# Kernel optimization log

Hardware: AMD Instinct MI355X
Metric: run time of the kernel (lower is better)

## Reference

```python
import jax, jax.numpy as jnp
import numpy as np

NUM_CLASSES = 100000
NUM_SAMPLED = 5000  # num_classes * cr, cr = 0.05
BATCH = 4096
DIM = 1024


def _log_expected_count(idx, num_sampled, num_classes):
    # TF LogUniformCandidateSampler: P(c) = log((c+2)/(c+1)) / log(num_classes+1)
    c = idx.astype(jnp.float32)
    p = jnp.log((c + 2.0) / (c + 1.0)) / jnp.log(float(num_classes) + 1.0)
    # expected count for unique sampling of num_sampled candidates
    return jnp.log(-jnp.expm1(num_sampled * jnp.log1p(-p)))


def setup_inputs() -> dict:
    key = jax.random.key(0)
    k1, k2, k3, k4 = jax.random.split(key, 4)
    x = jax.random.normal(k1, (BATCH, DIM), dtype=jnp.float32)
    w = jax.random.normal(k2, (DIM, NUM_CLASSES), dtype=jnp.float32) * 0.05  # tf random_normal_initializer stddev
    b = jnp.zeros((NUM_CLASSES,), dtype=jnp.float32)
    labels = jax.random.randint(k3, (BATCH,), 0, NUM_CLASSES)
    sampled = jax.random.randint(k4, (NUM_SAMPLED,), 0, NUM_CLASSES)
    return {"x": x, "w": w, "b": b, "labels": labels, "sampled": sampled}


def reference(x, w, b, labels, sampled):
    # sampled-class logits: gather columns of w then one small GEMM
    w_s = w[:, sampled]                                   # [D, S]
    sampled_logits = x @ w_s + b[sampled][None, :]        # [B, S]
    sampled_logits = sampled_logits - _log_expected_count(sampled, NUM_SAMPLED, NUM_CLASSES)[None, :]
    # true-class logit per example
    w_t = w[:, labels]                                    # [D, B]
    true_logits = jnp.einsum('bd,db->b', x, w_t) + b[labels]
    true_logits = true_logits - _log_expected_count(labels, NUM_SAMPLED, NUM_CLASSES)
    # softmax CE with true class in column 0 of [true | sampled]
    all_logits = jnp.concatenate([true_logits[:, None], sampled_logits], axis=1)  # [B, 1+S]
    loss = jnp.mean(jax.nn.logsumexp(all_logits, axis=1) - true_logits)
    return loss
```

## Files before the change

### kernel.cpp

```cpp
#include <hip/hip_runtime.h>
#include <hip/hip_bf16.h>

#define NUM_CLASSES 100000
#define NUM_SAMPLED 5000
#define BATCH 4096
#define DIM 1024
#define NPAD 5120

typedef float floatx4 __attribute__((ext_vector_type(4)));
typedef short bf16x8 __attribute__((ext_vector_type(8)));

__device__ __forceinline__ float log_expected_count(int c) {
    float p = log1pf(1.0f / (float)(c + 1)) / logf((float)NUM_CLASSES + 1.0f);
    float t = (float)NUM_SAMPLED * log1pf(-p);
    return logf(-expm1f(t));
}

__device__ __forceinline__ void async_ld16(const void* g, void* l) {
    __builtin_amdgcn_global_load_lds(
        (const __attribute__((address_space(1))) unsigned int*)g,
        (__attribute__((address_space(3))) unsigned int*)l,
        16, 0, 0);
}

__global__ __launch_bounds__(256) void init_kernel(float* rowsum) {
    int i = blockIdx.x * 256 + threadIdx.x;
    if (i < BATCH) rowsum[i] = 0.0f;
}

__global__ __launch_bounds__(256) void convert_x_kernel(const float* __restrict__ x,
                                                        __hip_bfloat16* __restrict__ A) {
    int i = (blockIdx.x * 256 + threadIdx.x) * 4;
    float4 v = *reinterpret_cast<const float4*>(x + i);
    union { ushort4 u; __hip_bfloat16 h[4]; } o;
    o.h[0] = __float2bfloat16(v.x);
    o.h[1] = __float2bfloat16(v.y);
    o.h[2] = __float2bfloat16(v.z);
    o.h[3] = __float2bfloat16(v.w);
    *reinterpret_cast<ushort4*>(A + i) = o.u;
}

__global__ __launch_bounds__(256) void gather_b_kernel(const float* __restrict__ w,
                                                       const float* __restrict__ b,
                                                       const int* __restrict__ sampled,
                                                       __hip_bfloat16* __restrict__ BT,
                                                       float* __restrict__ shift) {
    int n  = blockIdx.x * 256 + threadIdx.x;
    int k0 = blockIdx.y * 16;
    bool valid = (n < NUM_SAMPLED);
    int c = valid ? sampled[n] : 0;
    if (blockIdx.y == 0) {
        shift[n] = valid ? (b[c] - log_expected_count(c)) : -1e30f;
    }
    __hip_bfloat16* dst = BT + (size_t)n * DIM + k0;
    if (valid) {
        const float* src = w + (size_t)k0 * NUM_CLASSES + c;
        #pragma unroll
        for (int kk = 0; kk < 16; kk += 8) {
            union { uint4 u; __hip_bfloat16 h[8]; } o;
            #pragma unroll
            for (int j = 0; j < 8; j++)
                o.h[j] = __float2bfloat16(src[(size_t)(kk + j) * NUM_CLASSES]);
            *reinterpret_cast<uint4*>(dst + kk) = o.u;
        }
    } else {
        uint4 z; z.x = z.y = z.z = z.w = 0u;
        #pragma unroll
        for (int kk = 0; kk < 16; kk += 8)
            *reinterpret_cast<uint4*>(dst + kk) = z;
    }
}

#define BM 128
#define BN 128
#define BK 64

__global__ __launch_bounds__(256) void gemm_kernel(const __hip_bfloat16* __restrict__ A,
                                                   const __hip_bfloat16* __restrict__ BT,
                                                   const float* __restrict__ shift,
                                                   float* __restrict__ rowsum) {
    __shared__ __hip_bfloat16 As[BM * BK];
    __shared__ __hip_bfloat16 Bs[BN * BK];

    const int tid  = threadIdx.x;
    const int m0   = blockIdx.x * BM;
    const int n0   = blockIdx.y * BN;
    const int lane = tid & 63;
    const int wv   = tid >> 6;
    const int wm   = (wv >> 1) * 64;
    const int wn   = (wv & 1) * 64;
    const int col  = lane & 15;
    const int quad = lane >> 4;

    floatx4 acc[4][4] = {};

    const __hip_bfloat16* gA[4];
    const __hip_bfloat16* gB[4];
    int ldsOff[4];
    #pragma unroll
    for (int r = 0; r < 4; r++) {
        int eo  = tid * 8 + r * 2048;
        int row = eo >> 6;
        int cl  = eo & 63;
        gA[r] = A  + (size_t)(m0 + row) * DIM + cl;
        gB[r] = BT + (size_t)(n0 + row) * DIM + cl;
        ldsOff[r] = eo;
    }

    for (int kt = 0; kt < DIM; kt += BK) {
        #pragma unroll
        for (int r = 0; r < 4; r++)
            async_ld16(gA[r] + kt, &As[ldsOff[r]]);
        #pragma unroll
        for (int r = 0; r < 4; r++)
            async_ld16(gB[r] + kt, &Bs[ldsOff[r]]);
        __syncthreads();

        #pragma unroll
        for (int ks = 0; ks < 2; ks++) {
            const int kc = ks * 32 + quad * 8;
            bf16x8 af[4], bfr[4];
            #pragma unroll
            for (int i = 0; i < 4; i++) {
                af[i]  = *reinterpret_cast<const bf16x8*>(&As[(wm + i * 16 + col) * BK + kc]);
                bfr[i] = *reinterpret_cast<const bf16x8*>(&Bs[(wn + i * 16 + col) * BK + kc]);
            }
            #pragma unroll
            for (int i = 0; i < 4; i++)
                #pragma unroll
                for (int j = 0; j < 4; j++)
                    acc[i][j] = __builtin_amdgcn_mfma_f32_16x16x32_bf16(af[i], bfr[j], acc[i][j], 0, 0, 0);
        }
        __syncthreads();
    }

    float sh[4];
    #pragma unroll
    for (int j = 0; j < 4; j++)
        sh[j] = shift[n0 + wn + j * 16 + col];

    #pragma unroll
    for (int i = 0; i < 4; i++) {
        #pragma unroll
        for (int r = 0; r < 4; r++) {
            float s = 0.0f;
            #pragma unroll
            for (int j = 0; j < 4; j++)
                s += __expf(acc[i][j][r] + sh[j]);
            s += __shfl_xor(s, 1);
            s += __shfl_xor(s, 2);
            s += __shfl_xor(s, 4);
            s += __shfl_xor(s, 8);
            if (col == 0) {
                int mrow = m0 + wm + i * 16 + quad * 4 + r;
                atomicAdd(&rowsum[mrow], s);
            }
        }
    }
}

__global__ __launch_bounds__(256) void rowloss_kernel(const float* __restrict__ x,
                                                      const float* __restrict__ w,
                                                      const float* __restrict__ b,
                                                      const int* __restrict__ labels,
                                                      const float* __restrict__ rowsum,
                                                      float* __restrict__ rowloss) {
    __shared__ float red[4];
    const int m = blockIdx.x;
    const int t = threadIdx.x;
    const int lbl = labels[m];
    const float* xr = x + (size_t)m * DIM;
    const float* wc = w + lbl;

    float p = 0.0f;
    #pragma unroll
    for (int d = t; d < DIM; d += 256)
        p += xr[d] * wc[(size_t)d * NUM_CLASSES];

    #pragma unroll
    for (int off = 32; off > 0; off >>= 1)
        p += __shfl_xor(p, off);
    if ((t & 63) == 0) red[t >> 6] = p;
    __syncthreads();
    if (t == 0) {
        float tl = red[0] + red[1] + red[2] + red[3] + b[lbl] - log_expected_count(lbl);
        float total = rowsum[m] + __expf(tl);
        rowloss[m] = logf(total) - tl;
    }
}

__global__ __launch_bounds__(256) void reduce_kernel(const float* __restrict__ rowloss,
                                                     float* __restrict__ out) {
    __shared__ float red[4];
    const int t = threadIdx.x;
    float s = 0.0f;
    #pragma unroll
    for (int i = t; i < BATCH; i += 256)
        s += rowloss[i];
    #pragma unroll
    for (int off = 32; off > 0; off >>= 1)
        s += __shfl_xor(s, off);
    if ((t & 63) == 0) red[t >> 6] = s;
    __syncthreads();
    if (t == 0)
        out[0] = (red[0] + red[1] + red[2] + red[3]) * (1.0f / (float)BATCH);
}

extern "C" void kernel_launch(void* const* d_in, const int* in_sizes, int n_in,
                              void* d_out, int out_size, void* d_ws, size_t ws_size,
                              hipStream_t stream) {
    const float* x       = (const float*)d_in[0];
    const float* w       = (const float*)d_in[1];
    const float* b       = (const float*)d_in[2];
    const int*   labels  = (const int*)d_in[3];
    const int*   sampled = (const int*)d_in[4];
    float* out = (float*)d_out;

    char* ws = (char*)d_ws;
    __hip_bfloat16* A  = (__hip_bfloat16*)(ws);
    __hip_bfloat16* BT = (__hip_bfloat16*)(ws + (size_t)8  * 1024 * 1024);
    float* shift   = (float*)(ws + (size_t)18 * 1024 * 1024);
    float* rowsum  = (float*)(ws + (size_t)18 * 1024 * 1024 + 64 * 1024);
    float* rowloss = (float*)(ws + (size_t)18 * 1024 * 1024 + 128 * 1024);

    hipLaunchKernelGGL(init_kernel, dim3(16), dim3(256), 0, stream, rowsum);
    hipLaunchKernelGGL(convert_x_kernel, dim3((BATCH * DIM / 4) / 256), dim3(256), 0, stream, x, A);
    hipLaunchKernelGGL(gather_b_kernel, dim3(NPAD / 256, DIM / 16), dim3(256), 0, stream,
                       w, b, sampled, BT, shift);
    hipLaunchKernelGGL(gemm_kernel, dim3(BATCH / BM, NPAD / BN), dim3(256), 0, stream,
                       A, BT, shift, rowsum);
    hipLaunchKernelGGL(rowloss_kernel, dim3(BATCH), dim3(256), 0, stream,
                       x, w, b, labels, rowsum, rowloss);
    hipLaunchKernelGGL(reduce_kernel, dim3(1), dim3(256), 0, stream, rowloss, out);
}
```

Baseline: 720.4 us.

## Replace strided column gathers with coalesced scan of w plus dedup map

Builds class-to-first-index maps for the sampled and label classes, then streams the whole weight matrix row-wise with coalesced float4 loads. Only the columns that are needed are scattered into bf16 transposed buffers for the sampled and label columns, and a fixup kernel copies rows for duplicate classes. This is meant to remove the uncoalesced per-element strided column gathers in the gather and rowloss kernels. The cost is reading all of w (about 400MB), three extra small kernels, and a true-class dot product that now runs in bf16 instead of fp32.

Result: slower. 895.4 us (+24.3%).

```diff
diff --git a/kernel.cpp b/kernel.cpp
--- a/kernel.cpp
+++ b/kernel.cpp
@@ -23,9 +23,41 @@
         16, 0, 0);
 }
 
-__global__ __launch_bounds__(256) void init_kernel(float* rowsum) {
+__global__ __launch_bounds__(256) void init_kernel(int* map_s, int* map_l, float* rowsum) {
     int i = blockIdx.x * 256 + threadIdx.x;
+    if (i < NUM_CLASSES) { map_s[i] = 0x7FFFFFFF; map_l[i] = 0x7FFFFFFF; }
     if (i < BATCH) rowsum[i] = 0.0f;
+}
+
+__global__ __launch_bounds__(256) void build_kernel(const float* __restrict__ b,
+                                                    const int* __restrict__ sampled,
+                                                    const int* __restrict__ labels,
+                                                    int* map_s, int* map_l,
+                                                    float* __restrict__ shift) {
+    int id = blockIdx.x * 256 + threadIdx.x;
+    if (id < NPAD) {
+        if (id < NUM_SAMPLED) {
+            int c = sampled[id];
+            atomicMin(&map_s[c], id);
+            shift[id] = b[c] - log_expected_count(c);
+        } else {
+            shift[id] = -1e30f;
+        }
+    } else if (id < NPAD + BATCH) {
+        int m = id - NPAD;
+        atomicMin(&map_l[labels[m]], m);
+    }
+}
+
+__global__ __launch_bounds__(256) void pack_kernel(const int* __restrict__ map_s,
+                                                   const int* __restrict__ map_l,
+                                                   int* __restrict__ packed) {
+    int i = blockIdx.x * 256 + threadIdx.x;
+    if (i < NUM_CLASSES) {
+        unsigned s = (unsigned)min(map_s[i], 0xFFFF);
+        unsigned l = (unsigned)min(map_l[i], 0xFFFF);
+        packed[i] = (int)(s | (l << 16));
+    }
 }
 
 __global__ __launch_bounds__(256) void convert_x_kernel(const float* __restrict__ x,
@@ -40,34 +72,77 @@
     *reinterpret_cast<ushort4*>(A + i) = o.u;
 }
 
-__global__ __launch_bounds__(256) void gather_b_kernel(const float* __restrict__ w,
-                                                       const float* __restrict__ b,
-                                                       const int* __restrict__ sampled,
-                                                       __hip_bfloat16* __restrict__ BT,
-                                                       float* __restrict__ shift) {
-    int n  = blockIdx.x * 256 + threadIdx.x;
-    int k0 = blockIdx.y * 16;
-    bool valid = (n < NUM_SAMPLED);
-    int c = valid ? sampled[n] : 0;
-    if (blockIdx.y == 0) {
-        shift[n] = valid ? (b[c] - log_expected_count(c)) : -1e30f;
-    }
-    __hip_bfloat16* dst = BT + (size_t)n * DIM + k0;
-    if (valid) {
-        const float* src = w + (size_t)k0 * NUM_CLASSES + c;
-        #pragma unroll
-        for (int kk = 0; kk < 16; kk += 8) {
-            union { uint4 u; __hip_bfloat16 h[8]; } o;
+__global__ __launch_bounds__(256) void scan_kernel(const float* __restrict__ w,
+                                                   const int* __restrict__ packed,
+                                                   __hip_bfloat16* __restrict__ BT,
+                                                   __hip_bfloat16* __restrict__ LBT) {
+    const int c  = blockIdx.x * 1024 + threadIdx.x * 4;
+    const int k0 = blockIdx.y * 32;
+    if (c >= NUM_CLASSES) return;
+    const bool full = (c + 3 < NUM_CLASSES);
+
+    unsigned pk[4];
+    if (full) {
+        int4 p = *reinterpret_cast<const int4*>(packed + c);
+        pk[0] = (unsigned)p.x; pk[1] = (unsigned)p.y;
+        pk[2] = (unsigned)p.z; pk[3] = (unsigned)p.w;
+    } else {
+        #pragma unroll
+        for (int j = 0; j < 4; j++)
+            pk[j] = (c + j < NUM_CLASSES) ? (unsigned)packed[c + j] : 0xFFFFFFFFu;
+    }
+
+    int sd[4], ld[4];
+    bool any = false;
+    #pragma unroll
+    for (int j = 0; j < 4; j++) {
+        unsigned s = pk[j] & 0xFFFFu;
+        unsigned l = pk[j] >> 16;
+        sd[j] = (s != 0xFFFFu) ? (int)s : -1;
+        ld[j] = (l != 0xFFFFu) ? (int)l : -1;
+        any |= (sd[j] >= 0) | (ld[j] >= 0);
+    }
+    if (!any) return;
+
+    for (int k = 0; k < 32; k++) {
+        const size_t rowoff = (size_t)(k0 + k) * NUM_CLASSES;
+        float vv[4];
+        if (full) {
+            float4 v = *reinterpret_cast<const float4*>(w + rowoff + c);
+            vv[0] = v.x; vv[1] = v.y; vv[2] = v.z; vv[3] = v.w;
+        } else {
             #pragma unroll
-            for (int j = 0; j < 8; j++)
-                o.h[j] = __float2bfloat16(src[(size_t)(kk + j) * NUM_CLASSES]);
-            *reinterpret_cast<uint4*>(dst + kk) = o.u;
-        }
-    } else {
-        uint4 z; z.x = z.y = z.z = z.w = 0u;
-        #pragma unroll
-        for (int kk = 0; kk < 16; kk += 8)
-            *reinterpret_cast<uint4*>(dst + kk) = z;
+            for (int j = 0; j < 4; j++)
+                vv[j] = (c + j < NUM_CLASSES) ? w[rowoff + c + j] : 0.0f;
+        }
+        #pragma unroll
+        for (int j = 0; j < 4; j++) {
+            if (sd[j] >= 0) BT [(size_t)sd[j] * DIM + k0 + k] = __float2bfloat16(vv[j]);
+            if (ld[j] >= 0) LBT[(size_t)ld[j] * DIM + k0 + k] = __float2bfloat16(vv[j]);
+        }
+    }
+}
+
+__global__ __launch_bounds__(256) void dupfix_kernel(const int* __restrict__ sampled,
+                                                     const int* __restrict__ labels,
+                                                     const int* __restrict__ packed,
+                                                     __hip_bfloat16* __restrict__ BT,
+                                                     __hip_bfloat16* __restrict__ LBT) {
+    const int wid  = blockIdx.x * 4 + (threadIdx.x >> 6);
+    const int lane = threadIdx.x & 63;
+    const __hip_bfloat16* src = nullptr;
+    __hip_bfloat16* dst = nullptr;
+    if (wid < NUM_SAMPLED) {
+        unsigned f = (unsigned)packed[sampled[wid]] & 0xFFFFu;
+        if ((int)f != wid) { src = BT + (size_t)f * DIM; dst = BT + (size_t)wid * DIM; }
+    } else if (wid < NUM_SAMPLED + BATCH) {
+        int m = wid - NUM_SAMPLED;
+        unsigned f = (unsigned)packed[labels[m]] >> 16;
+        if ((int)f != m) { src = LBT + (size_t)f * DIM; dst = LBT + (size_t)m * DIM; }
+    }
+    if (dst) {
+        reinterpret_cast<uint4*>(dst)[lane]      = reinterpret_cast<const uint4*>(src)[lane];
+        reinterpret_cast<uint4*>(dst)[lane + 64] = reinterpret_cast<const uint4*>(src)[lane + 64];
     }
 }
 
@@ -159,33 +234,36 @@
     }
 }
 
-__global__ __launch_bounds__(256) void rowloss_kernel(const float* __restrict__ x,
-                                                      const float* __restrict__ w,
+__global__ __launch_bounds__(256) void rowloss_kernel(const __hip_bfloat16* __restrict__ A,
+                                                      const __hip_bfloat16* __restrict__ LBT,
                                                       const float* __restrict__ b,
                                                       const int* __restrict__ labels,
                                                       const float* __restrict__ rowsum,
                                                       float* __restrict__ rowloss) {
-    __shared__ float red[4];
-    const int m = blockIdx.x;
-    const int t = threadIdx.x;
-    const int lbl = labels[m];
-    const float* xr = x + (size_t)m * DIM;
-    const float* wc = w + lbl;
+    const int m    = blockIdx.x * 4 + (threadIdx.x >> 6);
+    const int lane = threadIdx.x & 63;
+    const size_t base = (size_t)m * DIM + lane * 8;
 
     float p = 0.0f;
     #pragma unroll
-    for (int d = t; d < DIM; d += 256)
-        p += xr[d] * wc[(size_t)d * NUM_CLASSES];
-
+    for (int h = 0; h < 2; h++) {
+        bf16x8 av = *reinterpret_cast<const bf16x8*>(A   + base + h * 512);
+        bf16x8 lv = *reinterpret_cast<const bf16x8*>(LBT + base + h * 512);
+        #pragma unroll
+        for (int j = 0; j < 8; j++) {
+            union { short s; __hip_bfloat16 h16; } ua, ul;
+            ua.s = av[j]; ul.s = lv[j];
+            p = fmaf(__bfloat162float(ua.h16), __bfloat162float(ul.h16), p);
+        }
+    }
     #pragma unroll
     for (int off = 32; off > 0; off >>= 1)
         p += __shfl_xor(p, off);
-    if ((t & 63) == 0) red[t >> 6] = p;
-    __syncthreads();
-    if (t == 0) {
-        float tl = red[0] + red[1] + red[2] + red[3] + b[lbl] - log_expected_count(lbl);
-        float total = rowsum[m] + __expf(tl);
-        rowloss[m] = logf(total) - tl;
+
+    if (lane == 0) {
+        int lbl = labels[m];
+        float tl = p + b[lbl] - log_expected_count(lbl);
+        rowloss[m] = logf(rowsum[m] + __expf(tl)) - tl;
     }
 }
 
@@ -217,19 +295,31 @@
     float* out = (float*)d_out;
 
     char* ws = (char*)d_ws;
-    __hip_bfloat16* A  = (__hip_bfloat16*)(ws);
-    __hip_bfloat16* BT = (__hip_bfloat16*)(ws + (size_t)8  * 1024 * 1024);
-    float* shift   = (float*)(ws + (size_t)18 * 1024 * 1024);
-    float* rowsum  = (float*)(ws + (size_t)18 * 1024 * 1024 + 64 * 1024);
-    float* rowloss = (float*)(ws + (size_t)18 * 1024 * 1024 + 128 * 1024);
-
-    hipLaunchKernelGGL(init_kernel, dim3(16), dim3(256), 0, stream, rowsum);
+    const size_t MB = 1024 * 1024;
+    __hip_bfloat16* A      = (__hip_bfloat16*)(ws);
+    __hip_bfloat16* BT     = (__hip_bfloat16*)(ws + 8  * MB);
+    __hip_bfloat16* LBT    = (__hip_bfloat16*)(ws + 18 * MB);
+    int*   packed  = (int*)  (ws + 26 * MB);
+    int*   map_s   = (int*)  (ws + 27 * MB);
+    int*   map_l   = (int*)  (ws + 28 * MB);
+    float* shift   = (float*)(ws + 29 * MB);
+    float* rowsum  = (float*)(ws + 29 * MB + 64 * 1024);
+    float* rowloss = (float*)(ws + 29 * MB + 128 * 1024);
+
+    hipLaunchKernelGGL(init_kernel, dim3((NUM_CLASSES + 255) / 256), dim3(256), 0, stream,
+                       map_s, map_l, rowsum);
+    hipLaunchKernelGGL(build_kernel, dim3((NPAD + BATCH + 255) / 256), dim3(256), 0, stream,
+                       b, sampled, labels, map_s, map_l, shift);
+    hipLaunchKernelGGL(pack_kernel, dim3((NUM_CLASSES + 255) / 256), dim3(256), 0, stream,
+                       map_s, map_l, packed);
     hipLaunchKernelGGL(convert_x_kernel, dim3((BATCH * DIM / 4) / 256), dim3(256), 0, stream, x, A);
-    hipLaunchKernelGGL(gather_b_kernel, dim3(NPAD / 256, DIM / 16), dim3(256), 0, stream,
-                       w, b, sampled, BT, shift);
+    hipLaunchKernelGGL(scan_kernel, dim3((NUM_CLASSES + 1023) / 1024, DIM / 32), dim3(256), 0, stream,
+                       w, packed, BT, LBT);
+    hipLaunchKernelGGL(dupfix_kernel, dim3((NUM_SAMPLED + BATCH + 3) / 4), dim3(256), 0, stream,
+                       sampled, labels, packed, BT, LBT);
     hipLaunchKernelGGL(gemm_kernel, dim3(BATCH / BM, NPAD / BN), dim3(256), 0, stream,
                        A, BT, shift, rowsum);
-    hipLaunchKernelGGL(rowloss_kernel, dim3(BATCH), dim3(256), 0, stream,
-                       x, w, b, labels, rowsum, rowloss);
+    hipLaunchKernelGGL(rowloss_kernel, dim3(BATCH / 4), dim3(256), 0, stream,
+                       A, LBT, b, labels, rowsum, rowloss);
     hipLaunchKernelGGL(reduce_kernel, dim3(1), dim3(256), 0, stream, rowloss, out);
 }
```
